# Kernel tuning notes

Measured on AMD Instinct MI355X. Metric: run time of the kernel, lower is better.

## Reference

```python
import jax, jax.numpy as jnp
import numpy as np

HEADS = 6
WIN = 7
SHIFT = 3
NEG = -100.0


def _rel_index():
    # Swin relative position index, [49, 49] int
    coords = np.stack(np.meshgrid(np.arange(WIN), np.arange(WIN), indexing='ij')).reshape(2, -1)
    rel = (coords[:, :, None] - coords[:, None, :]).transpose(1, 2, 0)
    rel[:, :, 0] += WIN - 1
    rel[:, :, 1] += WIN - 1
    rel[:, :, 0] *= 2 * WIN - 1
    return rel.sum(-1)


def _shift_mask(H, W):
    # additive shift mask per window, [num_windows, 49, 49]
    img = np.zeros([H, W])
    slices = (slice(0, -WIN), slice(-WIN, -SHIFT), slice(-SHIFT, None))
    cnt = 0
    for h in slices:
        for w in slices:
            img[h, w] = cnt
            cnt += 1
    mw = img.reshape(H // WIN, WIN, W // WIN, WIN).transpose(0, 2, 1, 3).reshape(-1, WIN * WIN)
    diff = mw[:, None, :] - mw[:, :, None]
    return np.where(diff != 0, NEG, 0.0).astype(np.float32)


def setup_inputs() -> dict:
    key = jax.random.key(0)
    ks = jax.random.split(key, 6)
    B, H, W, C = 64, 56, 56, 192
    return {
        'x': jax.random.normal(ks[0], (B, H, W, C), jnp.float32),
        'qkv_w': jax.random.normal(ks[1], (C, 3 * C), jnp.float32) * 0.02,
        'qkv_b': jax.random.normal(ks[2], (3 * C,), jnp.float32) * 0.02,
        'rel_table': jax.random.normal(ks[3], ((2 * WIN - 1) ** 2, HEADS), jnp.float32) * 0.02,
        'proj_w': jax.random.normal(ks[4], (C, C), jnp.float32) * 0.02,
        'proj_b': jax.random.normal(ks[5], (C,), jnp.float32) * 0.02,
    }


def reference(x, qkv_w, qkv_b, rel_table, proj_w, proj_b):
    B, H, W, C = x.shape
    hd = C // HEADS
    scale = hd ** -0.5
    mask = jnp.asarray(_shift_mask(H, W))            # [nW, N, N]
    idx = _rel_index().reshape(-1)                   # static numpy [N*N]

    # cyclic shift + window partition
    xs = jnp.roll(x, (-SHIFT, -SHIFT), (1, 2))
    xw = xs.reshape(B, H // WIN, WIN, W // WIN, WIN, C)
    xw = xw.transpose(0, 1, 3, 2, 4, 5).reshape(-1, WIN * WIN, C)  # [Bn, N, C]
    Bn, N, _ = xw.shape

    qkv = (xw @ qkv_w + qkv_b).reshape(Bn, N, 3, HEADS, hd).transpose(2, 0, 3, 1, 4)
    q, k, v = qkv[0] * scale, qkv[1], qkv[2]         # [Bn, h, N, hd]

    attn = jax.nn.softmax(jnp.einsum('bhnd,bhmd->bhnm', q, k), axis=-1)

    # NOTE: original module adds relative bias and shift mask AFTER softmax
    bias = rel_table[idx].reshape(N, N, HEADS).transpose(2, 0, 1)  # [h, N, N]
    attn = attn + bias[None]
    nW = mask.shape[0]
    attn = (attn.reshape(Bn // nW, nW, HEADS, N, N) + mask[None, :, None]).reshape(Bn, HEADS, N, N)

    out = jnp.einsum('bhnm,bhmd->bhnd', attn, v).transpose(0, 2, 1, 3).reshape(Bn, N, C)
    out = out @ proj_w + proj_b

    # window reverse + un-shift
    out = out.reshape(B, H // WIN, W // WIN, WIN, WIN, C)
    out = out.transpose(0, 1, 3, 2, 4, 5).reshape(B, H, W, C)
    return jnp.roll(out, (SHIFT, SHIFT), (1, 2))
```

## Files before the change

kernel.cpp:

```cpp
#include <hip/hip_runtime.h>
#include <hip/hip_bf16.h>

typedef __attribute__((ext_vector_type(8))) short bf16x8_t;
typedef __attribute__((ext_vector_type(4))) short bf16x4_t;
typedef __attribute__((ext_vector_type(4))) float f32x4_t;

#define MFMA16 __builtin_amdgcn_mfma_f32_16x16x32_bf16

#if __has_builtin(__builtin_amdgcn_mfma_f32_16x16x16bf16_1k)
#define HAVE_MFMA_K16 1
#define MFMA16K16 __builtin_amdgcn_mfma_f32_16x16x16bf16_1k
#else
#define HAVE_MFMA_K16 0
#endif

__device__ __forceinline__ unsigned short f2bf(float f) {
    return __builtin_bit_cast(unsigned short, __float2bfloat16(f));
}
__device__ __forceinline__ int cvt_pk_bf16(float lo, float hi) {
    int r;
    asm("v_cvt_pk_bf16_f32 %0, %1, %2" : "=v"(r) : "v"(lo), "v"(hi));
    return r;
}

__device__ __forceinline__ void group_barrier(int* cnt, int target, int ln) {
    asm volatile("s_waitcnt lgkmcnt(0)" ::: "memory");
    if (ln == 0)
        __hip_atomic_fetch_add(cnt, 1, __ATOMIC_RELEASE, __HIP_MEMORY_SCOPE_WORKGROUP);
    while (__hip_atomic_load(cnt, __ATOMIC_ACQUIRE, __HIP_MEMORY_SCOPE_WORKGROUP) < target)
        __builtin_amdgcn_s_sleep(1);
    __builtin_amdgcn_sched_barrier(0);
}

#define XB_OFF     98304
#define ROWOFF_OFF 149504
#define BAR_OFF    150528
#define SMEM_BYTES 150536

__device__ __forceinline__ int qk_byte(int row, int d) {
    return row * 64 + ((((d >> 3) ^ ((row >> 1) & 3)) << 4) | ((d & 7) << 1));
}
__device__ __forceinline__ int vt_byte(int d, int tok) {
    return d * 128 + ((((tok >> 3) ^ (d & 7)) << 4) | ((tok & 7) << 1));
}

__global__ void prep_weights(const float* __restrict__ qkv_w, const float* __restrict__ proj_w,
                             unsigned short* __restrict__ wqkvT, unsigned short* __restrict__ wprojT)
{
    int i = blockIdx.x * 256 + threadIdx.x;
    if (i < 576 * 192) {
        int n = i / 192, k = i - n * 192;
        wqkvT[i] = f2bf(qkv_w[k * 576 + n]);
    }
    if (i < 192 * 192) {
        int n = i / 192, k = i - n * 192;
        wprojT[i] = f2bf(proj_w[k * 192 + n]);
    }
}

__global__ void prep_bias(const float* __restrict__ rel_table, float* __restrict__ biasT)
{
    int i = blockIdx.x * 256 + threadIdx.x;
    if (i >= 4 * 6 * 16 * 64) return;
    int ln  = i & 63;
    int f   = (i >> 6) & 15;
    int h   = (i >> 10) % 6;
    int wt  = i / 6144;
    int l15 = ln & 15, lg = ln >> 4;
    int mk  = f >> 2, nq = f & 3;
    int qt  = nq * 16 + l15;
    bool bh = (wt & 2) != 0, bw = (wt & 1) != 0;
    float4 o = {0.f, 0.f, 0.f, 0.f};
    float* po = (float*)&o;
    int iq = qt / 7, jq = qt - iq * 7;
    int regq = (bh ? ((iq < 4) ? 3 : 6) : 0) + (bw ? ((jq < 4) ? 1 : 2) : 0);
    for (int r = 0; r < 4; ++r) {
        int kt = mk * 16 + lg * 4 + r;
        if (kt < 49 && qt < 49) {
            int ik = kt / 7, jk = kt - ik * 7;
            int idx = (iq - ik + 6) * 13 + (jq - jk + 6);
            int regk = (bh ? ((ik < 4) ? 3 : 6) : 0) + (bw ? ((jk < 4) ? 1 : 2) : 0);
            po[r] = rel_table[idx * 6 + h] + ((regk != regq) ? -100.0f : 0.0f);
        }
    }
    ((float4*)biasT)[i] = o;
}

__global__ __launch_bounds__(768, 3)
void swin_fused(const float* __restrict__ x,
                const float* __restrict__ qkv_b,
                const float* __restrict__ proj_b,
                const unsigned short* __restrict__ wqkvT,
                const unsigned short* __restrict__ wprojT,
                const float* __restrict__ biasT,
                float* __restrict__ out)
{
    __shared__ unsigned char smem[SMEM_BYTES];

    const int tid = threadIdx.x;
    const int wv  = tid >> 6;
    const int g   = (wv >= 6) ? 1 : 0;
    const int h   = wv - 6 * g;
    const int ln  = tid & 63;
    const int l15 = ln & 15;
    const int lg  = ln >> 4;
    const int tg  = tid - g * 384;

    const int bw  = blockIdx.x * 2 + g;
    const int b   = bw >> 6;
    const int win = bw & 63;
    const int wh  = win >> 3;
    const int ww  = win & 7;
    const int wt  = ((wh == 7) ? 2 : 0) | ((ww == 7) ? 1 : 0);

    const unsigned gbase = g * 49152;
    const unsigned hbase = gbase + h * 8192;
    const unsigned xb    = XB_OFF + g * 25600;
    int* rowOff = (int*)(smem + ROWOFF_OFF + g * 256);
    int* bar    = (int*)(smem + BAR_OFF) + g;
    const f32x4_t zero4 = {0.f, 0.f, 0.f, 0.f};

    if (tid < 2) ((int*)(smem + BAR_OFF))[tid] = 0;
    __syncthreads();

    if (g == 1) {
        while (__hip_atomic_load((int*)(smem + BAR_OFF), __ATOMIC_ACQUIRE,
                                 __HIP_MEMORY_SCOPE_WORKGROUP) < 6)
            __builtin_amdgcn_s_sleep(2);
        __builtin_amdgcn_sched_barrier(0);
    }

#pragma unroll
    for (int it = 0; it < 8; ++it) {
        int idx = tg + it * 384;
        int n   = idx / 48;
        int c4  = idx - n * 48;
        int2* dst = (int2*)(smem + xb + n * 400 + c4 * 8);
        if (n < 49) {
            int i = n / 7, j = n - i * 7;
            int sh = wh * 7 + i + 3; if (sh >= 56) sh -= 56;
            int sw = ww * 7 + j + 3; if (sw >= 56) sw -= 56;
            int ro = ((b * 56 + sh) * 56 + sw) * 192;
            if (c4 == 0) rowOff[n] = ro;
            const float4* src = (const float4*)(x + ro + c4 * 4);
            float4 v = *src;
            int2 p;
            p.x = cvt_pk_bf16(v.x, v.y);
            p.y = cvt_pk_bf16(v.z, v.w);
            *dst = p;
        } else {
            *dst = make_int2(0, 0);
        }
    }
    group_barrier(bar, 6, ln);

    f32x4_t accq[4][6];
#pragma unroll
    for (int mt = 0; mt < 4; ++mt)
#pragma unroll
        for (int nt = 0; nt < 6; ++nt) accq[mt][nt] = zero4;
#pragma unroll
    for (int ks = 0; ks < 6; ++ks) {
        bf16x8_t af[4];
#pragma unroll
        for (int mt = 0; mt < 4; ++mt)
            af[mt] = *(const bf16x8_t*)(smem + xb + (mt * 16 + l15) * 400 + (ks * 32 + lg * 8) * 2);
        bf16x8_t bfv[6];
#pragma unroll
        for (int nt = 0; nt < 6; ++nt)
            bfv[nt] = *(const bf16x8_t*)(wqkvT + ((nt >> 1) * 192 + h * 32 + (nt & 1) * 16 + l15) * 192 + ks * 32 + lg * 8);
        __builtin_amdgcn_s_setprio(1);
#pragma unroll
        for (int nt = 0; nt < 6; ++nt)
#pragma unroll
            for (int mt = 0; mt < 4; ++mt)
                accq[mt][nt] = MFMA16(af[mt], bfv[nt], accq[mt][nt], 0, 0, 0);
        __builtin_amdgcn_s_setprio(0);
    }
    int vbf[4][2][2];
#pragma unroll
    for (int nv = 0; nv < 2; ++nv) {
        float bb = qkv_b[384 + h * 32 + nv * 16 + l15];
#pragma unroll
        for (int mt = 0; mt < 4; ++mt) {
            vbf[mt][nv][0] = cvt_pk_bf16(accq[mt][4 + nv][0] + bb, accq[mt][4 + nv][1] + bb);
            vbf[mt][nv][1] = cvt_pk_bf16(accq[mt][4 + nv][2] + bb, accq[mt][4 + nv][3] + bb);
        }
    }

#pragma unroll
    for (int nt = 0; nt < 4; ++nt) {
        int part = nt >> 1;
        int d    = (nt & 1) * 16 + l15;
        float bb = qkv_b[part * 192 + h * 32 + d];
        unsigned base = hbase + part * 4096;
#pragma unroll
        for (int mt = 0; mt < 4; ++mt)
#pragma unroll
            for (int r = 0; r < 4; ++r) {
                int row = mt * 16 + lg * 4 + r;
                *(unsigned short*)(smem + base + qk_byte(row, d)) = f2bf(accq[mt][nt][r] + bb);
            }
    }
    __builtin_amdgcn_sched_barrier(0);

    f32x4_t s[4][4];
    {
        bf16x8_t kf[4], qf[4];
#pragma unroll
        for (int mk = 0; mk < 4; ++mk) {
            int row = mk * 16 + l15;
            kf[mk] = *(const bf16x8_t*)(smem + hbase + 4096 + row * 64 + ((lg ^ ((row >> 1) & 3)) << 4));
        }
#pragma unroll
        for (int nq = 0; nq < 4; ++nq) {
            int row = nq * 16 + l15;
            qf[nq] = *(const bf16x8_t*)(smem + hbase + row * 64 + ((lg ^ ((row >> 1) & 3)) << 4));
        }
        __builtin_amdgcn_s_setprio(1);
#pragma unroll
        for (int mk = 0; mk < 4; ++mk)
#pragma unroll
            for (int nq = 0; nq < 4; ++nq)
                s[mk][nq] = MFMA16(kf[mk], qf[nq], zero4, 0, 0, 0);
        __builtin_amdgcn_s_setprio(0);
    }
    __builtin_amdgcn_sched_barrier(0);

#pragma unroll
    for (int nv = 0; nv < 2; ++nv) {
        int d = nv * 16 + l15;
#pragma unroll
        for (int mt = 0; mt < 4; ++mt) {
            int tok = mt * 16 + lg * 4;
            *(int2*)(smem + hbase + vt_byte(d, tok)) = make_int2(vbf[mt][nv][0], vbf[mt][nv][1]);
        }
    }

    float4 bv4[4][4];
    {
        const float4* bp = (const float4*)biasT + (wt * 6 + h) * 16 * 64 + ln;
#pragma unroll
        for (int mk = 0; mk < 4; ++mk)
#pragma unroll
            for (int nq = 0; nq < 4; ++nq)
                bv4[mk][nq] = bp[(mk * 4 + nq) * 64];
    }

    const float C = 0.17677669529663687f * 1.4426950408889634f;
    int w[4][4][2];
#pragma unroll
    for (int nq = 0; nq < 4; ++nq) {
        float sum = 0.f;
#pragma unroll
        for (int mk = 0; mk < 4; ++mk)
#pragma unroll
            for (int r = 0; r < 4; ++r) {
                int kt = mk * 16 + lg * 4 + r;
                float e = (kt < 49) ? __builtin_amdgcn_exp2f(C * s[mk][nq][r]) : 0.0f;
                s[mk][nq][r] = e;
                sum += e;
            }
        sum += __shfl_xor(sum, 16);
        sum += __shfl_xor(sum, 32);
        float inv = __builtin_amdgcn_rcpf(sum);
#pragma unroll
        for (int mk = 0; mk < 4; ++mk) {
            float v0 = fmaf(s[mk][nq][0], inv, bv4[mk][nq].x);
            float v1 = fmaf(s[mk][nq][1], inv, bv4[mk][nq].y);
            float v2 = fmaf(s[mk][nq][2], inv, bv4[mk][nq].z);
            float v3 = fmaf(s[mk][nq][3], inv, bv4[mk][nq].w);
            w[mk][nq][0] = cvt_pk_bf16(v0, v1);
            w[mk][nq][1] = cvt_pk_bf16(v2, v3);
        }
    }

    f32x4_t o[2][4];
#pragma unroll
    for (int md = 0; md < 2; ++md)
#pragma unroll
        for (int nq = 0; nq < 4; ++nq) o[md][nq] = zero4;

#if HAVE_MFMA_K16
#pragma unroll
    for (int mk = 0; mk < 4; ++mk) {
        bf16x4_t vt2[2];
#pragma unroll
        for (int md = 0; md < 2; ++md) {
            int d = md * 16 + l15;
            vt2[md] = *(const bf16x4_t*)(smem + hbase + vt_byte(d, mk * 16 + lg * 4));
        }
        __builtin_amdgcn_s_setprio(1);
#pragma unroll
        for (int nq = 0; nq < 4; ++nq) {
            bf16x4_t wb = __builtin_bit_cast(bf16x4_t, make_int2(w[mk][nq][0], w[mk][nq][1]));
#pragma unroll
            for (int md = 0; md < 2; ++md)
                o[md][nq] = MFMA16K16(vt2[md], wb, o[md][nq], 0, 0, 0);
        }
        __builtin_amdgcn_s_setprio(0);
    }
#else
    const unsigned Abase = hbase + 4096;
#pragma unroll
    for (int ks = 0; ks < 2; ++ks) {
#pragma unroll
        for (int mh = 0; mh < 2; ++mh) {
            int mk = ks * 2 + mh;
            int d  = mh * 16 + lg * 4;
#pragma unroll
            for (int nq = 0; nq < 4; ++nq) {
                int qt = nq * 16 + l15;
                *(int2*)(smem + Abase + qk_byte(qt, d)) = make_int2(w[mk][nq][0], w[mk][nq][1]);
            }
        }
        __builtin_amdgcn_sched_barrier(0);
        bf16x8_t vf[2], bfr[4];
#pragma unroll
        for (int md = 0; md < 2; ++md) {
            int d = md * 16 + l15;
            vf[md] = *(const bf16x8_t*)(smem + hbase + d * 128 + (((ks * 4 + lg) ^ (d & 7)) << 4));
        }
#pragma unroll
        for (int nq = 0; nq < 4; ++nq) {
            int qt = nq * 16 + l15;
            bfr[nq] = *(const bf16x8_t*)(smem + Abase + qt * 64 + ((lg ^ ((qt >> 1) & 3)) << 4));
        }
        __builtin_amdgcn_s_setprio(1);
#pragma unroll
        for (int nq = 0; nq < 4; ++nq)
#pragma unroll
            for (int md = 0; md < 2; ++md)
                o[md][nq] = MFMA16(vf[md], bfr[nq], o[md][nq], 0, 0, 0);
        __builtin_amdgcn_s_setprio(0);
        __builtin_amdgcn_sched_barrier(0);
    }
#endif
    group_barrier(bar, 12, ln);

#pragma unroll
    for (int md = 0; md < 2; ++md)
#pragma unroll
        for (int nq = 0; nq < 4; ++nq) {
            int qt = nq * 16 + l15;
            int ch = h * 32 + md * 16 + lg * 4;
            int d0 = cvt_pk_bf16(o[md][nq][0], o[md][nq][1]);
            int d1 = cvt_pk_bf16(o[md][nq][2], o[md][nq][3]);
            *(int2*)(smem + gbase + qt * 400 + ch * 2) = make_int2(d0, d1);
        }
    group_barrier(bar, 18, ln);

    f32x4_t y[4][2];
#pragma unroll
    for (int mt = 0; mt < 4; ++mt) { y[mt][0] = zero4; y[mt][1] = zero4; }
#pragma unroll
    for (int ks = 0; ks < 6; ++ks) {
        bf16x8_t aa[4], bb[2];
#pragma unroll
        for (int mt = 0; mt < 4; ++mt)
            aa[mt] = *(const bf16x8_t*)(smem + gbase + (mt * 16 + l15) * 400 + (ks * 32 + lg * 8) * 2);
#pragma unroll
        for (int nt = 0; nt < 2; ++nt)
            bb[nt] = *(const bf16x8_t*)(wprojT + (h * 32 + nt * 16 + l15) * 192 + ks * 32 + lg * 8);
        __builtin_amdgcn_s_setprio(1);
#pragma unroll
        for (int mt = 0; mt < 4; ++mt)
#pragma unroll
            for (int nt = 0; nt < 2; ++nt)
                y[mt][nt] = MFMA16(aa[mt], bb[nt], y[mt][nt], 0, 0, 0);
        __builtin_amdgcn_s_setprio(0);
    }
    float pb0 = proj_b[h * 32 + l15];
    float pb1 = proj_b[h * 32 + 16 + l15];
#pragma unroll
    for (int mt = 0; mt < 4; ++mt)
#pragma unroll
        for (int r = 0; r < 4; ++r) {
            int row = mt * 16 + lg * 4 + r;
            if (row < 49) {
                int ro = rowOff[row];
                out[ro + h * 32 + l15]      = y[mt][0][r] + pb0;
                out[ro + h * 32 + 16 + l15] = y[mt][1][r] + pb1;
            }
        }
}

extern "C" void kernel_launch(void* const* d_in, const int* in_sizes, int n_in,
                              void* d_out, int out_size, void* d_ws, size_t ws_size,
                              hipStream_t stream) {
    const float* x         = (const float*)d_in[0];
    const float* qkv_w     = (const float*)d_in[1];
    const float* qkv_b     = (const float*)d_in[2];
    const float* rel_table = (const float*)d_in[3];
    const float* proj_w    = (const float*)d_in[4];
    const float* proj_b    = (const float*)d_in[5];
    float* out = (float*)d_out;

    unsigned short* wqkvT  = (unsigned short*)d_ws;
    unsigned short* wprojT = wqkvT + 576 * 192;
    float* biasT = (float*)((char*)d_ws + 294912);

    prep_weights<<<576, 256, 0, stream>>>(qkv_w, proj_w, wqkvT, wprojT);
    prep_bias<<<96, 256, 0, stream>>>(rel_table, biasT);
    swin_fused<<<2048, 768, 0, stream>>>(x, qkv_b, proj_b, wqkvT, wprojT, biasT, out);
}
```

Measured before the change: 255.7 us.

## Pipeline x staging with QKV GEMM row tiles and use block barriers

```diff
diff --git a/kernel.cpp b/kernel.cpp
--- a/kernel.cpp
+++ b/kernel.cpp
@@ -23,19 +23,9 @@
     return r;
 }
 
-__device__ __forceinline__ void group_barrier(int* cnt, int target, int ln) {
-    asm volatile("s_waitcnt lgkmcnt(0)" ::: "memory");
-    if (ln == 0)
-        __hip_atomic_fetch_add(cnt, 1, __ATOMIC_RELEASE, __HIP_MEMORY_SCOPE_WORKGROUP);
-    while (__hip_atomic_load(cnt, __ATOMIC_ACQUIRE, __HIP_MEMORY_SCOPE_WORKGROUP) < target)
-        __builtin_amdgcn_s_sleep(1);
-    __builtin_amdgcn_sched_barrier(0);
-}
-
 #define XB_OFF     98304
 #define ROWOFF_OFF 149504
-#define BAR_OFF    150528
-#define SMEM_BYTES 150536
+#define SMEM_BYTES 150016
 
 __device__ __forceinline__ int qk_byte(int row, int d) {
     return row * 64 + ((((d >> 3) ^ ((row >> 1) & 3)) << 4) | ((d & 7) << 1));
@@ -86,6 +76,51 @@
     ((float4*)biasT)[i] = o;
 }
 
+#define STAGE_ISSUE(IT, V, DST, HAS)                                              \
+    {                                                                             \
+        int idx_ = tg + (IT) * 384;                                               \
+        int n_   = idx_ / 48;                                                     \
+        int c4_  = idx_ - n_ * 48;                                                \
+        DST = xb + n_ * 400 + c4_ * 8;                                            \
+        HAS = (n_ < 49);                                                          \
+        if (HAS) {                                                                \
+            int i_ = n_ / 7, j_ = n_ - i_ * 7;                                    \
+            int sh_ = wh * 7 + i_ + 3; if (sh_ >= 56) sh_ -= 56;                  \
+            int sw_ = ww * 7 + j_ + 3; if (sw_ >= 56) sw_ -= 56;                  \
+            int ro_ = ((b * 56 + sh_) * 56 + sw_) * 192;                          \
+            if (c4_ == 0) rowOff[n_] = ro_;                                       \
+            V = *(const float4*)(x + ro_ + c4_ * 4);                              \
+        } else {                                                                  \
+            *(int2*)(smem + DST) = make_int2(0, 0);                               \
+        }                                                                         \
+    }
+#define STAGE_COMMIT(V, DST, HAS)                                                 \
+    if (HAS) {                                                                    \
+        int2 pk_;                                                                 \
+        pk_.x = cvt_pk_bf16(V.x, V.y);                                            \
+        pk_.y = cvt_pk_bf16(V.z, V.w);                                            \
+        *(int2*)(smem + DST) = pk_;                                               \
+    }
+
+#define QKV_MT(MT)                                                                \
+    {                                                                             \
+        _Pragma("unroll")                                                         \
+        for (int ks = 0; ks < 6; ++ks) {                                          \
+            bf16x8_t af = *(const bf16x8_t*)(smem + xb + ((MT) * 16 + l15) * 400  \
+                                             + (ks * 32 + lg * 8) * 2);           \
+            bf16x8_t bfv[6];                                                      \
+            _Pragma("unroll")                                                     \
+            for (int nt = 0; nt < 6; ++nt)                                        \
+                bfv[nt] = *(const bf16x8_t*)(wqkvT + ((nt >> 1) * 192 + h * 32    \
+                              + (nt & 1) * 16 + l15) * 192 + ks * 32 + lg * 8);   \
+            __builtin_amdgcn_s_setprio(1);                                        \
+            _Pragma("unroll")                                                     \
+            for (int nt = 0; nt < 6; ++nt)                                        \
+                accq[MT][nt] = MFMA16(af, bfv[nt], accq[MT][nt], 0, 0, 0);        \
+            __builtin_amdgcn_s_setprio(0);                                        \
+        }                                                                         \
+    }
+
 __global__ __launch_bounds__(768, 3)
 void swin_fused(const float* __restrict__ x,
                 const float* __restrict__ qkv_b,
@@ -117,66 +152,55 @@
     const unsigned hbase = gbase + h * 8192;
     const unsigned xb    = XB_OFF + g * 25600;
     int* rowOff = (int*)(smem + ROWOFF_OFF + g * 256);
-    int* bar    = (int*)(smem + BAR_OFF) + g;
     const f32x4_t zero4 = {0.f, 0.f, 0.f, 0.f};
 
-    if (tid < 2) ((int*)(smem + BAR_OFF))[tid] = 0;
-    __syncthreads();
-
-    if (g == 1) {
-        while (__hip_atomic_load((int*)(smem + BAR_OFF), __ATOMIC_ACQUIRE,
-                                 __HIP_MEMORY_SCOPE_WORKGROUP) < 6)
-            __builtin_amdgcn_s_sleep(2);
-        __builtin_amdgcn_sched_barrier(0);
-    }
-
-#pragma unroll
-    for (int it = 0; it < 8; ++it) {
-        int idx = tg + it * 384;
-        int n   = idx / 48;
-        int c4  = idx - n * 48;
-        int2* dst = (int2*)(smem + xb + n * 400 + c4 * 8);
-        if (n < 49) {
-            int i = n / 7, j = n - i * 7;
-            int sh = wh * 7 + i + 3; if (sh >= 56) sh -= 56;
-            int sw = ww * 7 + j + 3; if (sw >= 56) sw -= 56;
-            int ro = ((b * 56 + sh) * 56 + sw) * 192;
-            if (c4 == 0) rowOff[n] = ro;
-            const float4* src = (const float4*)(x + ro + c4 * 4);
-            float4 v = *src;
-            int2 p;
-            p.x = cvt_pk_bf16(v.x, v.y);
-            p.y = cvt_pk_bf16(v.z, v.w);
-            *dst = p;
-        } else {
-            *dst = make_int2(0, 0);
-        }
-    }
-    group_barrier(bar, 6, ln);
-
     f32x4_t accq[4][6];
 #pragma unroll
     for (int mt = 0; mt < 4; ++mt)
 #pragma unroll
         for (int nt = 0; nt < 6; ++nt) accq[mt][nt] = zero4;
-#pragma unroll
-    for (int ks = 0; ks < 6; ++ks) {
-        bf16x8_t af[4];
-#pragma unroll
-        for (int mt = 0; mt < 4; ++mt)
-            af[mt] = *(const bf16x8_t*)(smem + xb + (mt * 16 + l15) * 400 + (ks * 32 + lg * 8) * 2);
-        bf16x8_t bfv[6];
-#pragma unroll
-        for (int nt = 0; nt < 6; ++nt)
-            bfv[nt] = *(const bf16x8_t*)(wqkvT + ((nt >> 1) * 192 + h * 32 + (nt & 1) * 16 + l15) * 192 + ks * 32 + lg * 8);
-        __builtin_amdgcn_s_setprio(1);
-#pragma unroll
-        for (int nt = 0; nt < 6; ++nt)
-#pragma unroll
-            for (int mt = 0; mt < 4; ++mt)
-                accq[mt][nt] = MFMA16(af[mt], bfv[nt], accq[mt][nt], 0, 0, 0);
-        __builtin_amdgcn_s_setprio(0);
-    }
+
+    {
+        float4 va, vb_; unsigned da, db; bool ha, hb;
+        STAGE_ISSUE(0, va, da, ha);
+        STAGE_ISSUE(1, vb_, db, hb);
+        STAGE_COMMIT(va, da, ha);
+        STAGE_COMMIT(vb_, db, hb);
+    }
+    __syncthreads();
+
+    {
+        float4 va, vb_; unsigned da, db; bool ha, hb;
+        STAGE_ISSUE(2, va, da, ha);
+        STAGE_ISSUE(3, vb_, db, hb);
+        QKV_MT(0);
+        STAGE_COMMIT(va, da, ha);
+        STAGE_COMMIT(vb_, db, hb);
+    }
+    __syncthreads();
+
+    {
+        float4 va, vb_; unsigned da, db; bool ha, hb;
+        STAGE_ISSUE(4, va, da, ha);
+        STAGE_ISSUE(5, vb_, db, hb);
+        QKV_MT(1);
+        STAGE_COMMIT(va, da, ha);
+        STAGE_COMMIT(vb_, db, hb);
+    }
+    __syncthreads();
+
+    {
+        float4 va, vb_; unsigned da, db; bool ha, hb;
+        STAGE_ISSUE(6, va, da, ha);
+        STAGE_ISSUE(7, vb_, db, hb);
+        QKV_MT(2);
+        STAGE_COMMIT(va, da, ha);
+        STAGE_COMMIT(vb_, db, hb);
+    }
+    __syncthreads();
+
+    QKV_MT(3);
+
     int vbf[4][2][2];
 #pragma unroll
     for (int nv = 0; nv < 2; ++nv) {
@@ -336,7 +360,7 @@
         __builtin_amdgcn_sched_barrier(0);
     }
 #endif
-    group_barrier(bar, 12, ln);
+    __syncthreads();
 
 #pragma unroll
     for (int md = 0; md < 2; ++md)
@@ -348,7 +372,7 @@
             int d1 = cvt_pk_bf16(o[md][nq][2], o[md][nq][3]);
             *(int2*)(smem + gbase + qt * 400 + ch * 2) = make_int2(d0, d1);
         }
-    group_barrier(bar, 18, ln);
+    __syncthreads();
 
     f32x4_t y[4][2];
 #pragma unroll
```

Result: slower. 463.2 us (+81.1%).
